# Kernel tuning notes

Measured on AMD Instinct MI355X. Metric: run time of the kernel, lower is better.

Reference implementation:

```python
import jax, jax.numpy as jnp
import numpy as np

RADIUS = 0.2
NSAMPLE = 32
EPS = 1e-5  # BatchNorm2d default eps


def _bn_relu(x, g, b):
    # BatchNorm2d in training mode: per-channel stats over (B, S, nsample), biased var.
    m = x.mean(axis=(0, 1, 2))
    v = jnp.mean((x - m) ** 2, axis=(0, 1, 2))
    return jax.nn.relu((x - m) * jax.lax.rsqrt(v + EPS) * g + b)


def setup_inputs() -> dict:
    key = jax.random.key(0)
    ks = jax.random.split(key, 8)
    B, N, S = 8, 8192, 2048
    xyz = jax.random.uniform(ks[0], (B, 3, N), dtype=jnp.float32)          # unit cube
    points = jax.random.normal(ks[1], (B, 3, N), dtype=jnp.float32)
    fps_idx = jax.random.randint(ks[2], (B, S), 0, N, dtype=jnp.int32)
    W1 = jax.random.normal(ks[3], (64, 6), dtype=jnp.float32) * 0.1
    W2 = jax.random.normal(ks[4], (64, 64), dtype=jnp.float32) * 0.1
    W3 = jax.random.normal(ks[5], (128, 64), dtype=jnp.float32) * 0.1
    return dict(
        xyz=xyz, points=points, fps_idx=fps_idx,
        W1=W1, g1=jnp.ones((64,)), b1=jnp.zeros((64,)),
        W2=W2, g2=jnp.ones((64,)), b2=jnp.zeros((64,)),
        W3=W3, g3=jnp.ones((128,)), b3=jnp.zeros((128,)),
    )


def reference(xyz, points, fps_idx, W1, g1, b1, W2, g2, b2, W3, g3, b3):
    B, _, N = xyz.shape
    xyz_t = jnp.transpose(xyz, (0, 2, 1))            # [B,N,3]
    pts_t = jnp.transpose(points, (0, 2, 1))         # [B,N,D]
    # gather_operation: sampled centers
    new_xyz_t = jnp.take_along_axis(xyz_t, fps_idx[:, :, None], axis=1)  # [B,S,3]
    # ball query: first NSAMPLE points within radius; pad with first hit
    d2 = jnp.sum((new_xyz_t[:, :, None, :] - xyz_t[:, None, :, :]) ** 2, axis=-1)  # [B,S,N]
    keys = jnp.where(d2 <= RADIUS * RADIUS, jnp.arange(N, dtype=jnp.int32), N)
    neg_top, _ = jax.lax.top_k(-keys, NSAMPLE)       # smallest keys first
    idx = -neg_top                                   # [B,S,NSAMPLE]
    idx = jnp.where(idx < N, idx, idx[:, :, 0:1])    # pad empty slots with first hit (self always in-radius)
    bidx = jnp.arange(B)[:, None, None]
    grouped_xyz = xyz_t[bidx, idx]                   # [B,S,ns,3]
    rel = grouped_xyz - new_xyz_t[:, :, None, :]     # center-relative coords
    grouped_pts = pts_t[bidx, idx]                   # [B,S,ns,D]
    feat = jnp.concatenate([rel, grouped_pts], axis=-1)  # [B,S,ns,3+D]
    for W, g, b in ((W1, g1, b1), (W2, g2, b2), (W3, g3, b3)):
        feat = _bn_relu(jnp.einsum('bsnc,oc->bsno', feat, W), g, b)
    new_points = jnp.max(feat, axis=2)               # max over neighbors -> [B,S,C]
    return jnp.transpose(new_xyz_t, (0, 2, 1)), jnp.transpose(new_points, (0, 2, 1))
```

## Files before the change

### kernel.cpp

```cpp
#include <hip/hip_runtime.h>
#include <hip/hip_bf16.h>

#define BB_ 8
#define NN_ 8192
#define SS_ 2048
#define NS 32
#define C1 64
#define C2 64
#define C3 128
#define RAD2 0.04f
#define BN_EPS 1e-5f
#define M_TOT (BB_*SS_*NS)
#define INV_M (1.0f/524288.0f)
#define YSTR 34

typedef __attribute__((ext_vector_type(8))) short bf16x8;
typedef __attribute__((ext_vector_type(4))) float f32x4;

#define FBF_OFF 0
#define WPK_OFF 2097152
#define ST_OFF  2104320
#define GMM_OFF 2104832
#define X2_OFF  4201984
#define WS_NEED ((size_t)(4201984 + 16777216) * 4)

__device__ inline unsigned pkbf(float a, float b) {
    __hip_bfloat162 h = __float22bfloat162_rn(make_float2(a, b));
    unsigned r; __builtin_memcpy(&r, &h, 4); return r;
}
__device__ inline bf16x8 asfrag(uint4 v) { bf16x8 r; __builtin_memcpy(&r, &v, 16); return r; }
__device__ inline float bflo(unsigned u) { unsigned x = u << 16; float f; __builtin_memcpy(&f, &x, 4); return f; }
__device__ inline float bfhi(unsigned u) { unsigned x = u & 0xffff0000u; float f; __builtin_memcpy(&f, &x, 4); return f; }

__device__ inline void fin1_ch(const float* __restrict__ st, const float* __restrict__ W1,
                               const float* __restrict__ g, const float* __restrict__ bb,
                               int o, float* __restrict__ al, float* __restrict__ cl) {
    float w[6];
    #pragma unroll
    for (int i = 0; i < 6; ++i) w[i] = W1[o * 6 + i];
    float ms = 0.f;
    #pragma unroll
    for (int i = 0; i < 6; ++i) ms = fmaf(w[i], st[i], ms);
    float m = ms * INV_M;
    float e2 = 0.f;
    #pragma unroll
    for (int ci = 0; ci < 6; ++ci)
        #pragma unroll
        for (int d = 0; d < 6; ++d) {
            int lo = ci < d ? ci : d, hi = ci < d ? d : ci;
            int idx = 6 + lo * 6 - lo * (lo + 1) / 2 + hi;
            e2 = fmaf(w[ci] * w[d], st[idx], e2);
        }
    float var = e2 * INV_M - m * m;
    float ai = g[o] * (1.0f / sqrtf(var + BN_EPS));
    al[o] = ai;
    cl[o] = bb[o] - m * ai;
}

__device__ inline void fin_ch(const float* __restrict__ sum, const float* __restrict__ sq,
                              const float* __restrict__ g, const float* __restrict__ bb,
                              int o, float* __restrict__ al, float* __restrict__ cl) {
    float m = sum[o] * INV_M;
    float var = sq[o] * INV_M - m * m;
    float ai = g[o] * (1.0f / sqrtf(var + BN_EPS));
    al[o] = ai;
    cl[o] = bb[o] - m * ai;
}

__global__ void k_ballquery(const float* __restrict__ xyz, const float* __restrict__ pts,
                            const int* __restrict__ fps, uint4* __restrict__ fbf) {
    __shared__ int lidx[4][NS];
    int tid = threadIdx.x;
    int wave = (blockIdx.x * blockDim.x + tid) >> 6;
    int lane = tid & 63;
    int wslot = tid >> 6;
    int b = wave / SS_;
    const float* xb = xyz + (size_t)b * 3 * NN_;
    const float* pb = pts + (size_t)b * 3 * NN_;
    int ci = fps[wave];
    float cx = xb[ci], cy = xb[NN_ + ci], cz = xb[2 * NN_ + ci];

    float px = xb[lane], py = xb[NN_ + lane], pz = xb[2 * NN_ + lane];
    int found = 0;
    int first_i = -1;
    for (int base = 0; base < NN_; base += 64) {
        float xv = px, yv = py, zv = pz;
        int nb = (base + 64 < NN_) ? base + 64 : 0;
        px = xb[nb + lane]; py = xb[NN_ + nb + lane]; pz = xb[2 * NN_ + nb + lane];
        float dx = xv - cx, dy = yv - cy, dz = zv - cz;
        float d2 = __fadd_rn(__fadd_rn(__fmul_rn(dx, dx), __fmul_rn(dy, dy)), __fmul_rn(dz, dz));
        bool inr = d2 <= RAD2;
        unsigned long long mask = __ballot(inr);
        if (first_i < 0 && mask) first_i = base + __builtin_ctzll(mask);
        if (inr) {
            int pos = found + __popcll(mask & ((1ull << lane) - 1ull));
            if (pos < NS) lidx[wslot][pos] = base + lane;
        }
        found += __popcll(mask);
        if (found >= NS) break;
    }
    if (found > NS) found = NS;
    if (lane < NS) {
        int j = (lane < found) ? lidx[wslot][lane] : first_i;
        uint4 o;
        o.x = pkbf(xb[j] - cx,           xb[NN_ + j] - cy);
        o.y = pkbf(xb[2 * NN_ + j] - cz, pb[j]);
        o.z = pkbf(pb[NN_ + j],          pb[2 * NN_ + j]);
        o.w = 0u;
        fbf[(size_t)wave * NS + lane] = o;
    }
}

__global__ void k_pack(const float* __restrict__ W1, const float* __restrict__ W2,
                       const float* __restrict__ W3, uint4* __restrict__ wf,
                       float* __restrict__ st) {
    if (blockIdx.x == 7) { st[threadIdx.x] = 0.f; st[threadIdx.x + 256] = 0.f; return; }
    int t = blockIdx.x * 256 + threadIdx.x;
    int l = t & 63, p = l & 15, qd = l >> 4;
    float v[8];
    if (t < 256) {
        int mt = t >> 6;
        #pragma unroll
        for (int j = 0; j < 8; ++j)
            v[j] = (qd == 0 && j < 6) ? W1[(mt * 16 + p) * 6 + j] : 0.f;
    } else if (t < 768) {
        int fr = (t - 256) >> 6;
        int mt = fr >> 1, kf = fr & 1;
        #pragma unroll
        for (int j = 0; j < 8; ++j)
            v[j] = W2[(16 * mt + p) * 64 + kf * 32 + qd * 8 + j];
    } else {
        int fr = (t - 768) >> 6;
        int nt = fr >> 1, kf = fr & 1;
        #pragma unroll
        for (int j = 0; j < 8; ++j)
            v[j] = W3[(nt * 16 + p) * 64 + kf * 32 + qd * 8 + j];
    }
    uint4 o;
    o.x = pkbf(v[0], v[1]); o.y = pkbf(v[2], v[3]);
    o.z = pkbf(v[4], v[5]); o.w = pkbf(v[6], v[7]);
    wf[t] = o;
}

__global__ void k_p1(const uint4* __restrict__ fbf, float* __restrict__ st) {
    __shared__ float sacc[27];
    int tid = threadIdx.x;
    if (tid < 27) sacc[tid] = 0.f;
    __syncthreads();
    int gt = blockIdx.x * 256 + tid;
    float vals[27];
    #pragma unroll
    for (int i = 0; i < 27; ++i) vals[i] = 0.f;
    #pragma unroll 1
    for (int it = 0; it < M_TOT / 65536; ++it) {
        uint4 w = fbf[it * 65536 + gt];
        float f[6] = { bflo(w.x), bfhi(w.x), bflo(w.y), bfhi(w.y), bflo(w.z), bfhi(w.z) };
        #pragma unroll
        for (int c = 0; c < 6; ++c) vals[c] += f[c];
        int q = 6;
        #pragma unroll
        for (int c = 0; c < 6; ++c)
            #pragma unroll
            for (int d = c; d < 6; ++d) { vals[q] = fmaf(f[c], f[d], vals[q]); ++q; }
    }
    int lane = tid & 63;
    #pragma unroll
    for (int i = 0; i < 27; ++i) {
        float v = vals[i];
        #pragma unroll
        for (int d = 32; d; d >>= 1) v += __shfl_xor(v, d);
        if (lane == 0) atomicAdd(&sacc[i], v);
    }
    __syncthreads();
    if (tid < 27) atomicAdd(&st[tid], sacc[tid]);
}

__global__ __launch_bounds__(128) void k_p2(
        const uint4* __restrict__ fbf, const uint4* __restrict__ wpk,
        float* __restrict__ st,
        const float* __restrict__ W1, const float* __restrict__ g1, const float* __restrict__ b1,
        uint2* __restrict__ x2, int store_x2) {
    __shared__ unsigned yls[2][64 * YSTR];
    __shared__ float bs[C2], bq[C2];
    __shared__ float a1ls[C1], c1ls[C1];
    int tid = threadIdx.x, wslot = tid >> 6, lane = tid & 63;
    int p = lane & 15, qd = lane >> 4;
    if (tid < C2) { bs[tid] = 0.f; bq[tid] = 0.f; fin1_ch(st, W1, g1, b1, tid, a1ls, c1ls); }
    __syncthreads();
    const uint4* w1f = wpk;
    const uint4* w2f = wpk + 256;
    unsigned* my = yls[wslot];
    float s2[4][4], q2[4][4];
    #pragma unroll
    for (int i = 0; i < 4; ++i)
        #pragma unroll
        for (int r = 0; r < 4; ++r) { s2[i][r] = 0.f; q2[i][r] = 0.f; }

    #pragma unroll 1
    for (int it = 0; it < 4; ++it) {
        int tile = it * 2048 + blockIdx.x * 2 + wslot;
        int base = tile * 64;
        bf16x8 B1[4];
        #pragma unroll
        for (int nt = 0; nt < 4; ++nt) {
            uint4 v = make_uint4(0u, 0u, 0u, 0u);
            if (qd == 0) v = fbf[base + nt * 16 + p];
            B1[nt] = asfrag(v);
        }
        #pragma unroll
        for (int mt = 0; mt < 4; ++mt) {
            bf16x8 A = asfrag(w1f[mt * 64 + lane]);
            float4 av = *(const float4*)(a1ls + mt * 16 + qd * 4);
            float4 cv = *(const float4*)(c1ls + mt * 16 + qd * 4);
            #pragma unroll
            for (int nt = 0; nt < 4; ++nt) {
                f32x4 acc = {0.f, 0.f, 0.f, 0.f};
                acc = __builtin_amdgcn_mfma_f32_16x16x32_bf16(A, B1[nt], acc, 0, 0, 0);
                float y0 = fmaxf(fmaf(av.x, acc[0], cv.x), 0.f);
                float y1 = fmaxf(fmaf(av.y, acc[1], cv.y), 0.f);
                float y2 = fmaxf(fmaf(av.z, acc[2], cv.z), 0.f);
                float y3 = fmaxf(fmaf(av.w, acc[3], cv.w), 0.f);
                int a = (nt * 16 + p) * YSTR + mt * 8 + qd * 2;
                *(uint2*)&my[a] = make_uint2(pkbf(y0, y1), pkbf(y2, y3));
            }
        }
        __syncthreads();
        bf16x8 B2[4][2];
        #pragma unroll
        for (int nt = 0; nt < 4; ++nt)
            #pragma unroll
            for (int kf = 0; kf < 2; ++kf)
                B2[nt][kf] = asfrag(*(const uint4*)&my[(nt * 16 + p) * YSTR + kf * 16 + qd * 4]);
        #pragma unroll
        for (int mt = 0; mt < 4; ++mt) {
            f32x4 acc[4];
            #pragma unroll
            for (int nt = 0; nt < 4; ++nt) acc[nt] = (f32x4){0.f, 0.f, 0.f, 0.f};
            #pragma unroll
            for (int kf = 0; kf < 2; ++kf) {
                bf16x8 W = asfrag(w2f[(mt * 2 + kf) * 64 + lane]);
                #pragma unroll
                for (int nt = 0; nt < 4; ++nt)
                    acc[nt] = __builtin_amdgcn_mfma_f32_16x16x32_bf16(W, B2[nt][kf], acc[nt], 0, 0, 0);
            }
            if (store_x2) {
                #pragma unroll
                for (int nt = 0; nt < 4; ++nt)
                    x2[(size_t)(tile * 64 + nt * 16 + p) * 16 + mt * 4 + qd] =
                        make_uint2(pkbf(acc[nt][0], acc[nt][1]), pkbf(acc[nt][2], acc[nt][3]));
            }
            #pragma unroll
            for (int r = 0; r < 4; ++r) {
                float u0 = acc[0][r], u1 = acc[1][r], u2 = acc[2][r], u3 = acc[3][r];
                s2[mt][r] += (u0 + u1) + (u2 + u3);
                q2[mt][r] = fmaf(u0, u0, fmaf(u1, u1, fmaf(u2, u2, fmaf(u3, u3, q2[mt][r]))));
            }
        }
        __syncthreads();
    }
    #pragma unroll
    for (int mt = 0; mt < 4; ++mt)
        #pragma unroll
        for (int r = 0; r < 4; ++r) {
            float s = s2[mt][r], q = q2[mt][r];
            #pragma unroll
            for (int off = 1; off <= 8; off <<= 1) { s += __shfl_xor(s, off); q += __shfl_xor(q, off); }
            if (p == 0) {
                atomicAdd(&bs[mt * 16 + qd * 4 + r], s);
                atomicAdd(&bq[mt * 16 + qd * 4 + r], q);
            }
        }
    __syncthreads();
    if (tid < C2) { atomicAdd(&st[64 + tid], bs[tid]); atomicAdd(&st[128 + tid], bq[tid]); }
}

__global__ __launch_bounds__(256) void k_p3_l3(
        const uint2* __restrict__ x2, const uint4* __restrict__ wpk,
        float* __restrict__ st,
        const float* __restrict__ g2, const float* __restrict__ b2,
        const float* __restrict__ g3, float* __restrict__ gmm) {
    __shared__ uint4 w3ls[1024];
    __shared__ float bs[C3], bq[C3];
    __shared__ float a2ls[C2], c2ls[C2];
    int tid = threadIdx.x, wslot = tid >> 6, lane = tid & 63;
    int p = lane & 15, qd = lane >> 4;
    if (tid < 128) bs[tid] = 0.f; else bq[tid - 128] = 0.f;
    #pragma unroll
    for (int i = 0; i < 4; ++i) w3ls[i * 256 + tid] = wpk[768 + i * 256 + tid];
    if (tid < C2) fin_ch(st + 64, st + 128, g2, b2, tid, a2ls, c2ls);
    __syncthreads();
    const uint4* x2u4 = (const uint4*)x2;
    float a2r[2][8], c2r[2][8];
    #pragma unroll
    for (int kf = 0; kf < 2; ++kf)
        #pragma unroll
        for (int j = 0; j < 8; ++j) {
            a2r[kf][j] = a2ls[kf * 32 + qd * 8 + j];
            c2r[kf][j] = c2ls[kf * 32 + qd * 8 + j];
        }
    float gs3[8], gq3[8];
    bool pos[8];
    #pragma unroll
    for (int i = 0; i < 8; ++i) { gs3[i] = 0.f; gq3[i] = 0.f; pos[i] = g3[i * 16 + p] >= 0.f; }

    #pragma unroll 1
    for (int it = 0; it < 2; ++it) {
        int tile = it * 4096 + blockIdx.x * 4 + wslot;
        bf16x8 A3[4][2];
        #pragma unroll
        for (int mt = 0; mt < 4; ++mt)
            #pragma unroll
            for (int kf = 0; kf < 2; ++kf) {
                uint4 u = x2u4[(size_t)(tile * 64 + mt * 16 + p) * 8 + kf * 4 + qd];
                unsigned w[4] = { u.x, u.y, u.z, u.w };
                unsigned res[4];
                #pragma unroll
                for (int wi = 0; wi < 4; ++wi) {
                    float lo = bflo(w[wi]), hi = bfhi(w[wi]);
                    float ylo = fmaxf(fmaf(a2r[kf][2 * wi], lo, c2r[kf][2 * wi]), 0.f);
                    float yhi = fmaxf(fmaf(a2r[kf][2 * wi + 1], hi, c2r[kf][2 * wi + 1]), 0.f);
                    res[wi] = pkbf(ylo, yhi);
                }
                uint4 o;
                o.x = res[0]; o.y = res[1]; o.z = res[2]; o.w = res[3];
                A3[mt][kf] = asfrag(o);
            }
        #pragma unroll
        for (int nt = 0; nt < 8; ++nt) {
            bf16x8 Wa = asfrag(w3ls[(nt * 2 + 0) * 64 + lane]);
            bf16x8 Wb = asfrag(w3ls[(nt * 2 + 1) * 64 + lane]);
            f32x4 acc[4];
            #pragma unroll
            for (int mt = 0; mt < 4; ++mt) {
                acc[mt] = __builtin_amdgcn_mfma_f32_16x16x32_bf16(A3[mt][0], Wa,
                            (f32x4){0.f, 0.f, 0.f, 0.f}, 0, 0, 0);
                acc[mt] = __builtin_amdgcn_mfma_f32_16x16x32_bf16(A3[mt][1], Wb, acc[mt], 0, 0, 0);
            }
            float s = 0.f, q = 0.f, va = 0.f, vb = 0.f;
            #pragma unroll
            for (int mt = 0; mt < 4; ++mt) {
                float v0 = acc[mt][0], v1 = acc[mt][1], v2 = acc[mt][2], v3 = acc[mt][3];
                s += (v0 + v1) + (v2 + v3);
                q = fmaf(v0, v0, fmaf(v1, v1, fmaf(v2, v2, fmaf(v3, v3, q))));
                float mx = fmaxf(fmaxf(v0, v1), fmaxf(v2, v3));
                float mn = fminf(fminf(v0, v1), fminf(v2, v3));
                float vv = pos[nt] ? mx : -mn;
                if (mt == 0) va = vv;
                else if (mt == 1) va = fmaxf(va, vv);
                else if (mt == 2) vb = vv;
                else vb = fmaxf(vb, vv);
            }
            gs3[nt] += s; gq3[nt] += q;
            va = fmaxf(va, __shfl_xor(va, 16)); va = fmaxf(va, __shfl_xor(va, 32));
            vb = fmaxf(vb, __shfl_xor(vb, 16)); vb = fmaxf(vb, __shfl_xor(vb, 32));
            if (lane < 16) {
                gmm[(size_t)(tile * 2 + 0) * C3 + nt * 16 + lane] = va;
                gmm[(size_t)(tile * 2 + 1) * C3 + nt * 16 + lane] = vb;
            }
        }
    }
    #pragma unroll
    for (int nt = 0; nt < 8; ++nt) {
        float s = gs3[nt], q = gq3[nt];
        s += __shfl_xor(s, 16); s += __shfl_xor(s, 32);
        q += __shfl_xor(q, 16); q += __shfl_xor(q, 32);
        if (lane < 16) {
            atomicAdd(&bs[nt * 16 + lane], s);
            atomicAdd(&bq[nt * 16 + lane], q);
        }
    }
    __syncthreads();
    if (tid < C3) { atomicAdd(&st[192 + tid], bs[tid]); atomicAdd(&st[320 + tid], bq[tid]); }
}

__global__ __launch_bounds__(256) void k_p3_fused(
        const uint4* __restrict__ fbf, const uint4* __restrict__ wpk,
        float* __restrict__ st,
        const float* __restrict__ W1, const float* __restrict__ g1, const float* __restrict__ b1,
        const float* __restrict__ g2, const float* __restrict__ b2,
        const float* __restrict__ g3, float* __restrict__ gmm) {
    __shared__ unsigned yls[4][64 * YSTR];
    __shared__ uint4 w3ls[1024];
    __shared__ float bs[C3], bq[C3];
    __shared__ float a1ls[C1], c1ls[C1], a2ls[C2], c2ls[C2];
    int tid = threadIdx.x, wslot = tid >> 6, lane = tid & 63;
    int p = lane & 15, qd = lane >> 4;
    if (tid < 128) bs[tid] = 0.f; else bq[tid - 128] = 0.f;
    #pragma unroll
    for (int i = 0; i < 4; ++i) w3ls[i * 256 + tid] = wpk[768 + i * 256 + tid];
    if (tid < 64) fin1_ch(st, W1, g1, b1, tid, a1ls, c1ls);
    else if (tid < 128) fin_ch(st + 64, st + 128, g2, b2, tid - 64, a2ls, c2ls);
    __syncthreads();
    const uint4* w1f = wpk;
    const uint4* w2f = wpk + 256;
    unsigned* my = yls[wslot];
    float gs3[8], gq3[8];
    bool pos[8];
    #pragma unroll
    for (int i = 0; i < 8; ++i) { gs3[i] = 0.f; gq3[i] = 0.f; pos[i] = g3[i * 16 + p] >= 0.f; }

    #pragma unroll 1
    for (int it = 0; it < 2; ++it) {
        int tile = it * 4096 + blockIdx.x * 4 + wslot;
        int base = tile * 64;
        bf16x8 B1[4];
        #pragma unroll
        for (int nt = 0; nt < 4; ++nt) {
            uint4 v = make_uint4(0u, 0u, 0u, 0u);
            if (qd == 0) v = fbf[base + nt * 16 + p];
            B1[nt] = asfrag(v);
        }
        #pragma unroll
        for (int mt = 0; mt < 4; ++mt) {
            bf16x8 A = asfrag(w1f[mt * 64 + lane]);
            float4 av = *(const float4*)(a1ls + mt * 16 + qd * 4);
            float4 cv = *(const float4*)(c1ls + mt * 16 + qd * 4);
            #pragma unroll
            for (int nt = 0; nt < 4; ++nt) {
                f32x4 acc = {0.f, 0.f, 0.f, 0.f};
                acc = __builtin_amdgcn_mfma_f32_16x16x32_bf16(A, B1[nt], acc, 0, 0, 0);
                float y0 = fmaxf(fmaf(av.x, acc[0], cv.x), 0.f);
                float y1 = fmaxf(fmaf(av.y, acc[1], cv.y), 0.f);
                float y2 = fmaxf(fmaf(av.z, acc[2], cv.z), 0.f);
                float y3 = fmaxf(fmaf(av.w, acc[3], cv.w), 0.f);
                int a = (nt * 16 + p) * YSTR + mt * 8 + qd * 2;
                *(uint2*)&my[a] = make_uint2(pkbf(y0, y1), pkbf(y2, y3));
            }
        }
        __syncthreads();
        bf16x8 B2[4][2];
        #pragma unroll
        for (int nt = 0; nt < 4; ++nt)
            #pragma unroll
            for (int kf = 0; kf < 2; ++kf)
                B2[nt][kf] = asfrag(*(const uint4*)&my[(nt * 16 + p) * YSTR + kf * 16 + qd * 4]);
        __syncthreads();
        #pragma unroll
        for (int mt = 0; mt < 4; ++mt) {
            f32x4 acc[4];
            #pragma unroll
            for (int nt = 0; nt < 4; ++nt) acc[nt] = (f32x4){0.f, 0.f, 0.f, 0.f};
            #pragma unroll
            for (int kf = 0; kf < 2; ++kf) {
                bf16x8 W = asfrag(w2f[(mt * 2 + kf) * 64 + lane]);
                #pragma unroll
                for (int nt = 0; nt < 4; ++nt)
                    acc[nt] = __builtin_amdgcn_mfma_f32_16x16x32_bf16(W, B2[nt][kf], acc[nt], 0, 0, 0);
            }
            float4 av = *(const float4*)(a2ls + mt * 16 + qd * 4);
            float4 cv = *(const float4*)(c2ls + mt * 16 + qd * 4);
            #pragma unroll
            for (int nt = 0; nt < 4; ++nt) {
                float y0 = fmaxf(fmaf(av.x, acc[nt][0], cv.x), 0.f);
                float y1 = fmaxf(fmaf(av.y, acc[nt][1], cv.y), 0.f);
                float y2 = fmaxf(fmaf(av.z, acc[nt][2], cv.z), 0.f);
                float y3 = fmaxf(fmaf(av.w, acc[nt][3], cv.w), 0.f);
                int a = (nt * 16 + p) * YSTR + mt * 8 + qd * 2;
                *(uint2*)&my[a] = make_uint2(pkbf(y0, y1), pkbf(y2, y3));
            }
        }
        __syncthreads();
        bf16x8 A3[4][2];
        #pragma unroll
        for (int mt = 0; mt < 4; ++mt) {
            A3[mt][0] = asfrag(*(const uint4*)&my[(mt * 16 + p) * YSTR + qd * 4]);
            A3[mt][1] = asfrag(*(const uint4*)&my[(mt * 16 + p) * YSTR + 16 + qd * 4]);
        }
        __syncthreads();
        #pragma unroll
        for (int nt = 0; nt < 8; ++nt) {
            bf16x8 Wa = asfrag(w3ls[(nt * 2 + 0) * 64 + lane]);
            bf16x8 Wb = asfrag(w3ls[(nt * 2 + 1) * 64 + lane]);
            f32x4 acc[4];
            #pragma unroll
            for (int mt = 0; mt < 4; ++mt) {
                acc[mt] = __builtin_amdgcn_mfma_f32_16x16x32_bf16(A3[mt][0], Wa,
                            (f32x4){0.f, 0.f, 0.f, 0.f}, 0, 0, 0);
                acc[mt] = __builtin_amdgcn_mfma_f32_16x16x32_bf16(A3[mt][1], Wb, acc[mt], 0, 0, 0);
            }
            float s = 0.f, q = 0.f, va = 0.f, vb = 0.f;
            #pragma unroll
            for (int mt = 0; mt < 4; ++mt) {
                float v0 = acc[mt][0], v1 = acc[mt][1], v2 = acc[mt][2], v3 = acc[mt][3];
                s += (v0 + v1) + (v2 + v3);
                q = fmaf(v0, v0, fmaf(v1, v1, fmaf(v2, v2, fmaf(v3, v3, q))));
                float mx = fmaxf(fmaxf(v0, v1), fmaxf(v2, v3));
                float mn = fminf(fminf(v0, v1), fminf(v2, v3));
                float vv = pos[nt] ? mx : -mn;
                if (mt == 0) va = vv;
                else if (mt == 1) va = fmaxf(va, vv);
                else if (mt == 2) vb = vv;
                else vb = fmaxf(vb, vv);
            }
            gs3[nt] += s; gq3[nt] += q;
            va = fmaxf(va, __shfl_xor(va, 16)); va = fmaxf(va, __shfl_xor(va, 32));
            vb = fmaxf(vb, __shfl_xor(vb, 16)); vb = fmaxf(vb, __shfl_xor(vb, 32));
            if (lane < 16) {
                gmm[(size_t)(tile * 2 + 0) * C3 + nt * 16 + lane] = va;
                gmm[(size_t)(tile * 2 + 1) * C3 + nt * 16 + lane] = vb;
            }
        }
    }
    #pragma unroll
    for (int nt = 0; nt < 8; ++nt) {
        float s = gs3[nt], q = gq3[nt];
        s += __shfl_xor(s, 16); s += __shfl_xor(s, 32);
        q += __shfl_xor(q, 16); q += __shfl_xor(q, 32);
        if (lane < 16) {
            atomicAdd(&bs[nt * 16 + lane], s);
            atomicAdd(&bq[nt * 16 + lane], q);
        }
    }
    __syncthreads();
    if (tid < C3) { atomicAdd(&st[192 + tid], bs[tid]); atomicAdd(&st[320 + tid], bq[tid]); }
}

__global__ void k_outx(const float* __restrict__ gmm, const float* __restrict__ st,
                       const float* __restrict__ g3, const float* __restrict__ b3,
                       const float* __restrict__ xyz, const int* __restrict__ fps,
                       float* __restrict__ out) {
    __shared__ float T[C3][17];
    __shared__ float a3ls[C3], c3ls[C3];
    int blk = blockIdx.x, tid = threadIdx.x;
    if (blk < 1024) {
        if (tid < C3) fin_ch(st + 192, st + 320, g3, b3, tid, a3ls, c3ls);
        __syncthreads();
        int b = blk >> 7, s0 = (blk & 127) << 4;
        #pragma unroll
        for (int i = 0; i < 8; ++i) {
            int idx = i * 256 + tid;
            int sl = idx >> 7, o = idx & 127;
            float m = gmm[((size_t)(b * SS_ + s0 + sl)) * C3 + o];
            float a = a3ls[o];
            float v = (a >= 0.f) ? m : -m;
            T[o][sl] = fmaxf(fmaf(a, v, c3ls[o]), 0.f);
        }
        __syncthreads();
        int o = tid & 127, sh = tid >> 7;
        float* dst = out + (size_t)BB_ * 3 * SS_ + ((size_t)b * C3 + o) * SS_ + s0 + sh * 8;
        float4 w0, w1;
        w0.x = T[o][sh * 8 + 0]; w0.y = T[o][sh * 8 + 1];
        w0.z = T[o][sh * 8 + 2]; w0.w = T[o][sh * 8 + 3];
        w1.x = T[o][sh * 8 + 4]; w1.y = T[o][sh * 8 + 5];
        w1.z = T[o][sh * 8 + 6]; w1.w = T[o][sh * 8 + 7];
        *(float4*)dst = w0; *(float4*)(dst + 4) = w1;
    } else {
        int t = (blk - 1024) * 256 + tid;
        int b = t / (3 * SS_);
        int r = (t / SS_) % 3;
        int s = t % SS_;
        int ci = fps[b * SS_ + s];
        out[t] = xyz[((size_t)b * 3 + r) * NN_ + ci];
    }
}

extern "C" void kernel_launch(void* const* d_in, const int* in_sizes, int n_in,
                              void* d_out, int out_size, void* d_ws, size_t ws_size,
                              hipStream_t stream) {
    (void)in_sizes; (void)n_in; (void)out_size;
    const float* xyz = (const float*)d_in[0];
    const float* pts = (const float*)d_in[1];
    const int*   fps = (const int*)d_in[2];
    const float* W1 = (const float*)d_in[3];
    const float* g1 = (const float*)d_in[4];
    const float* b1 = (const float*)d_in[5];
    const float* W2 = (const float*)d_in[6];
    const float* g2 = (const float*)d_in[7];
    const float* b2 = (const float*)d_in[8];
    const float* W3 = (const float*)d_in[9];
    const float* g3 = (const float*)d_in[10];
    const float* b3 = (const float*)d_in[11];
    float* out = (float*)d_out;
    float* ws = (float*)d_ws;

    uint4* fbf = (uint4*)(ws + FBF_OFF);
    uint4* wpk = (uint4*)(ws + WPK_OFF);
    float* st  = ws + ST_OFF;
    float* gmm = ws + GMM_OFF;
    uint2* x2  = (uint2*)(ws + X2_OFF);
    int split = (ws_size >= WS_NEED) ? 1 : 0;

    k_pack<<<8, 256, 0, stream>>>(W1, W2, W3, wpk, st);
    k_ballquery<<<(BB_ * SS_) / 4, 256, 0, stream>>>(xyz, pts, fps, fbf);
    k_p1<<<256, 256, 0, stream>>>(fbf, st);
    k_p2<<<1024, 128, 0, stream>>>(fbf, wpk, st, W1, g1, b1, x2, split);
    if (split)
        k_p3_l3<<<1024, 256, 0, stream>>>(x2, wpk, st, g2, b2, g3, gmm);
    else
        k_p3_fused<<<1024, 256, 0, stream>>>(fbf, wpk, st, W1, g1, b1, g2, b2, g3, gmm);
    k_outx<<<1024 + 192, 256, 0, stream>>>(gmm, st, g3, b3, xyz, fps, out);
}
```

Baseline: 232.9 us.

## Fuse weight packing into ball query, double grids, and prefetch x2 rows in layer 3

Merges the weight-packing and stats-zeroing kernel into the ball-query kernel as extra blocks, which removes one launch. The p2 and p3_l3 kernels now launch twice as many blocks, each doing fewer tiles. In p3_l3 each wave handles one tile, loops over the 16-row groups, and software-prefetches the next group's x2 data, keeping running max registers instead of holding all A3 fragments at once. This cuts register pressure and raises parallelism, at the cost of more blocks doing per-block setup and atomics. One risk is that the stats-zeroing blocks now run concurrently with the ball query, but k_p1 is what consumes st, so ordering holds.

```diff
diff --git a/kernel.cpp b/kernel.cpp
--- a/kernel.cpp
+++ b/kernel.cpp
@@ -67,10 +67,43 @@
     cl[o] = bb[o] - m * ai;
 }
 
-__global__ void k_ballquery(const float* __restrict__ xyz, const float* __restrict__ pts,
-                            const int* __restrict__ fps, uint4* __restrict__ fbf) {
+__global__ void k_front(const float* __restrict__ xyz, const float* __restrict__ pts,
+                        const int* __restrict__ fps, uint4* __restrict__ fbf,
+                        const float* __restrict__ W1, const float* __restrict__ W2,
+                        const float* __restrict__ W3, uint4* __restrict__ wf,
+                        float* __restrict__ st) {
     __shared__ int lidx[4][NS];
     int tid = threadIdx.x;
+    if (blockIdx.x >= 4096) {
+        int bb = blockIdx.x - 4096;
+        if (bb == 7) { st[tid] = 0.f; st[tid + 256] = 0.f; return; }
+        int t = bb * 256 + tid;
+        int l = t & 63, p = l & 15, qd = l >> 4;
+        float v[8];
+        if (t < 256) {
+            int mt = t >> 6;
+            #pragma unroll
+            for (int j = 0; j < 8; ++j)
+                v[j] = (qd == 0 && j < 6) ? W1[(mt * 16 + p) * 6 + j] : 0.f;
+        } else if (t < 768) {
+            int fr = (t - 256) >> 6;
+            int mt = fr >> 1, kf = fr & 1;
+            #pragma unroll
+            for (int j = 0; j < 8; ++j)
+                v[j] = W2[(16 * mt + p) * 64 + kf * 32 + qd * 8 + j];
+        } else {
+            int fr = (t - 768) >> 6;
+            int nt = fr >> 1, kf = fr & 1;
+            #pragma unroll
+            for (int j = 0; j < 8; ++j)
+                v[j] = W3[(nt * 16 + p) * 64 + kf * 32 + qd * 8 + j];
+        }
+        uint4 o;
+        o.x = pkbf(v[0], v[1]); o.y = pkbf(v[2], v[3]);
+        o.z = pkbf(v[4], v[5]); o.w = pkbf(v[6], v[7]);
+        wf[t] = o;
+        return;
+    }
     int wave = (blockIdx.x * blockDim.x + tid) >> 6;
     int lane = tid & 63;
     int wslot = tid >> 6;
@@ -111,37 +144,6 @@
     }
 }
 
-__global__ void k_pack(const float* __restrict__ W1, const float* __restrict__ W2,
-                       const float* __restrict__ W3, uint4* __restrict__ wf,
-                       float* __restrict__ st) {
-    if (blockIdx.x == 7) { st[threadIdx.x] = 0.f; st[threadIdx.x + 256] = 0.f; return; }
-    int t = blockIdx.x * 256 + threadIdx.x;
-    int l = t & 63, p = l & 15, qd = l >> 4;
-    float v[8];
-    if (t < 256) {
-        int mt = t >> 6;
-        #pragma unroll
-        for (int j = 0; j < 8; ++j)
-            v[j] = (qd == 0 && j < 6) ? W1[(mt * 16 + p) * 6 + j] : 0.f;
-    } else if (t < 768) {
-        int fr = (t - 256) >> 6;
-        int mt = fr >> 1, kf = fr & 1;
-        #pragma unroll
-        for (int j = 0; j < 8; ++j)
-            v[j] = W2[(16 * mt + p) * 64 + kf * 32 + qd * 8 + j];
-    } else {
-        int fr = (t - 768) >> 6;
-        int nt = fr >> 1, kf = fr & 1;
-        #pragma unroll
-        for (int j = 0; j < 8; ++j)
-            v[j] = W3[(nt * 16 + p) * 64 + kf * 32 + qd * 8 + j];
-    }
-    uint4 o;
-    o.x = pkbf(v[0], v[1]); o.y = pkbf(v[2], v[3]);
-    o.z = pkbf(v[4], v[5]); o.w = pkbf(v[6], v[7]);
-    wf[t] = o;
-}
-
 __global__ void k_p1(const uint4* __restrict__ fbf, float* __restrict__ st) {
     __shared__ float sacc[27];
     int tid = threadIdx.x;
@@ -197,8 +199,8 @@
         for (int r = 0; r < 4; ++r) { s2[i][r] = 0.f; q2[i][r] = 0.f; }
 
     #pragma unroll 1
-    for (int it = 0; it < 4; ++it) {
-        int tile = it * 2048 + blockIdx.x * 2 + wslot;
+    for (int it = 0; it < 2; ++it) {
+        int tile = it * 4096 + blockIdx.x * 2 + wslot;
         int base = tile * 64;
         bf16x8 B1[4];
         #pragma unroll
@@ -298,65 +300,70 @@
             a2r[kf][j] = a2ls[kf * 32 + qd * 8 + j];
             c2r[kf][j] = c2ls[kf * 32 + qd * 8 + j];
         }
-    float gs3[8], gq3[8];
+    float gs3[8], gq3[8], va[8], vb[8];
     bool pos[8];
     #pragma unroll
-    for (int i = 0; i < 8; ++i) { gs3[i] = 0.f; gq3[i] = 0.f; pos[i] = g3[i * 16 + p] >= 0.f; }
-
+    for (int i = 0; i < 8; ++i) {
+        gs3[i] = 0.f; gq3[i] = 0.f; va[i] = -3.4e38f; vb[i] = -3.4e38f;
+        pos[i] = g3[i * 16 + p] >= 0.f;
+    }
+    int tile = blockIdx.x * 4 + wslot;
+    size_t pb = (size_t)tile * 64;
+
+    uint4 c0 = x2u4[(pb + p) * 8 + qd];
+    uint4 c1 = x2u4[(pb + p) * 8 + 4 + qd];
     #pragma unroll 1
-    for (int it = 0; it < 2; ++it) {
-        int tile = it * 4096 + blockIdx.x * 4 + wslot;
-        bf16x8 A3[4][2];
-        #pragma unroll
-        for (int mt = 0; mt < 4; ++mt)
-            #pragma unroll
-            for (int kf = 0; kf < 2; ++kf) {
-                uint4 u = x2u4[(size_t)(tile * 64 + mt * 16 + p) * 8 + kf * 4 + qd];
-                unsigned w[4] = { u.x, u.y, u.z, u.w };
-                unsigned res[4];
-                #pragma unroll
-                for (int wi = 0; wi < 4; ++wi) {
-                    float lo = bflo(w[wi]), hi = bfhi(w[wi]);
-                    float ylo = fmaxf(fmaf(a2r[kf][2 * wi], lo, c2r[kf][2 * wi]), 0.f);
-                    float yhi = fmaxf(fmaf(a2r[kf][2 * wi + 1], hi, c2r[kf][2 * wi + 1]), 0.f);
-                    res[wi] = pkbf(ylo, yhi);
-                }
-                uint4 o;
-                o.x = res[0]; o.y = res[1]; o.z = res[2]; o.w = res[3];
-                A3[mt][kf] = asfrag(o);
-            }
+    for (int mt = 0; mt < 4; ++mt) {
+        uint4 n0 = c0, n1 = c1;
+        if (mt < 3) {
+            n0 = x2u4[(pb + (mt + 1) * 16 + p) * 8 + qd];
+            n1 = x2u4[(pb + (mt + 1) * 16 + p) * 8 + 4 + qd];
+        }
+        bf16x8 A0, A1;
+        {
+            unsigned w0[4] = { c0.x, c0.y, c0.z, c0.w };
+            unsigned w1[4] = { c1.x, c1.y, c1.z, c1.w };
+            unsigned r0[4], r1[4];
+            #pragma unroll
+            for (int wi = 0; wi < 4; ++wi) {
+                float lo0 = bflo(w0[wi]), hi0 = bfhi(w0[wi]);
+                r0[wi] = pkbf(fmaxf(fmaf(a2r[0][2 * wi], lo0, c2r[0][2 * wi]), 0.f),
+                              fmaxf(fmaf(a2r[0][2 * wi + 1], hi0, c2r[0][2 * wi + 1]), 0.f));
+                float lo1 = bflo(w1[wi]), hi1 = bfhi(w1[wi]);
+                r1[wi] = pkbf(fmaxf(fmaf(a2r[1][2 * wi], lo1, c2r[1][2 * wi]), 0.f),
+                              fmaxf(fmaf(a2r[1][2 * wi + 1], hi1, c2r[1][2 * wi + 1]), 0.f));
+            }
+            uint4 t0 = make_uint4(r0[0], r0[1], r0[2], r0[3]);
+            uint4 t1 = make_uint4(r1[0], r1[1], r1[2], r1[3]);
+            A0 = asfrag(t0); A1 = asfrag(t1);
+        }
+        int g = mt >> 1;
         #pragma unroll
         for (int nt = 0; nt < 8; ++nt) {
             bf16x8 Wa = asfrag(w3ls[(nt * 2 + 0) * 64 + lane]);
             bf16x8 Wb = asfrag(w3ls[(nt * 2 + 1) * 64 + lane]);
-            f32x4 acc[4];
-            #pragma unroll
-            for (int mt = 0; mt < 4; ++mt) {
-                acc[mt] = __builtin_amdgcn_mfma_f32_16x16x32_bf16(A3[mt][0], Wa,
+            f32x4 acc = __builtin_amdgcn_mfma_f32_16x16x32_bf16(A0, Wa,
                             (f32x4){0.f, 0.f, 0.f, 0.f}, 0, 0, 0);
-                acc[mt] = __builtin_amdgcn_mfma_f32_16x16x32_bf16(A3[mt][1], Wb, acc[mt], 0, 0, 0);
-            }
-            float s = 0.f, q = 0.f, va = 0.f, vb = 0.f;
-            #pragma unroll
-            for (int mt = 0; mt < 4; ++mt) {
-                float v0 = acc[mt][0], v1 = acc[mt][1], v2 = acc[mt][2], v3 = acc[mt][3];
-                s += (v0 + v1) + (v2 + v3);
-                q = fmaf(v0, v0, fmaf(v1, v1, fmaf(v2, v2, fmaf(v3, v3, q))));
-                float mx = fmaxf(fmaxf(v0, v1), fmaxf(v2, v3));
-                float mn = fminf(fminf(v0, v1), fminf(v2, v3));
-                float vv = pos[nt] ? mx : -mn;
-                if (mt == 0) va = vv;
-                else if (mt == 1) va = fmaxf(va, vv);
-                else if (mt == 2) vb = vv;
-                else vb = fmaxf(vb, vv);
-            }
-            gs3[nt] += s; gq3[nt] += q;
-            va = fmaxf(va, __shfl_xor(va, 16)); va = fmaxf(va, __shfl_xor(va, 32));
-            vb = fmaxf(vb, __shfl_xor(vb, 16)); vb = fmaxf(vb, __shfl_xor(vb, 32));
-            if (lane < 16) {
-                gmm[(size_t)(tile * 2 + 0) * C3 + nt * 16 + lane] = va;
-                gmm[(size_t)(tile * 2 + 1) * C3 + nt * 16 + lane] = vb;
-            }
+            acc = __builtin_amdgcn_mfma_f32_16x16x32_bf16(A1, Wb, acc, 0, 0, 0);
+            float v0 = acc[0], v1 = acc[1], v2 = acc[2], v3 = acc[3];
+            gs3[nt] += (v0 + v1) + (v2 + v3);
+            gq3[nt] = fmaf(v0, v0, fmaf(v1, v1, fmaf(v2, v2, fmaf(v3, v3, gq3[nt]))));
+            float mx = fmaxf(fmaxf(v0, v1), fmaxf(v2, v3));
+            float mn = fminf(fminf(v0, v1), fminf(v2, v3));
+            float vv = pos[nt] ? mx : -mn;
+            if (g == 0) va[nt] = fmaxf(va[nt], vv);
+            else        vb[nt] = fmaxf(vb[nt], vv);
+        }
+        c0 = n0; c1 = n1;
+    }
+    #pragma unroll
+    for (int nt = 0; nt < 8; ++nt) {
+        float x = va[nt], y = vb[nt];
+        x = fmaxf(x, __shfl_xor(x, 16)); x = fmaxf(x, __shfl_xor(x, 32));
+        y = fmaxf(y, __shfl_xor(y, 16)); y = fmaxf(y, __shfl_xor(y, 32));
+        if (lane < 16) {
+            gmm[(size_t)(tile * 2 + 0) * C3 + nt * 16 + lane] = x;
+            gmm[(size_t)(tile * 2 + 1) * C3 + nt * 16 + lane] = y;
         }
     }
     #pragma unroll
@@ -580,12 +587,11 @@
     uint2* x2  = (uint2*)(ws + X2_OFF);
     int split = (ws_size >= WS_NEED) ? 1 : 0;
 
-    k_pack<<<8, 256, 0, stream>>>(W1, W2, W3, wpk, st);
-    k_ballquery<<<(BB_ * SS_) / 4, 256, 0, stream>>>(xyz, pts, fps, fbf);
+    k_front<<<4096 + 8, 256, 0, stream>>>(xyz, pts, fps, fbf, W1, W2, W3, wpk, st);
     k_p1<<<256, 256, 0, stream>>>(fbf, st);
-    k_p2<<<1024, 128, 0, stream>>>(fbf, wpk, st, W1, g1, b1, x2, split);
+    k_p2<<<2048, 128, 0, stream>>>(fbf, wpk, st, W1, g1, b1, x2, split);
     if (split)
-        k_p3_l3<<<1024, 256, 0, stream>>>(x2, wpk, st, g2, b2, g3, gmm);
+        k_p3_l3<<<2048, 256, 0, stream>>>(x2, wpk, st, g2, b2, g3, gmm);
     else
         k_p3_fused<<<1024, 256, 0, stream>>>(fbf, wpk, st, W1, g1, b1, g2, b2, g3, gmm);
     k_outx<<<1024 + 192, 256, 0, stream>>>(gmm, st, g3, b3, xyz, fps, out);
```

After: 261.1 us. 12.1% more time.
